# Optimization experiments

Measured on AMD Instinct MI355X. Metric: run time of the kernel, lower is better.

## Reference

```python
import jax, jax.numpy as jnp
import numpy as np

B, L, C = 8, 1_000_000, 4


def _spiral_size(length: int) -> int:
    # size = round(sqrt(L / (pi/4 * 0.7)) / 2) * 2 + 1  (odd, size^2 >= L)
    s = np.sqrt(length / (np.pi / 4.0 * 0.7))
    return int(np.round(s / 2.0)) * 2 + 1


def _spiral_perm(size: int, length: int):
    """Grid slot index for each signal position (first `length` of argsort(phi2))."""
    PI = jnp.float32(np.pi)
    rnge = jnp.arange(size, dtype=jnp.float32) - size / 2.0 + 0.5
    x1, x2 = jnp.meshgrid(rnge, rnge)  # 'xy' indexing, same as tf.meshgrid default
    r = jnp.sqrt(x1 * x1 + x2 * x2)
    phi = jnp.arccos(x1 / r)                      # NaN at center (0/0)
    phi = jnp.where(jnp.isnan(phi), 0.0, phi)
    phi = phi * jnp.sign(x2)
    phi = phi + jnp.where((x2 == 0.0) & (x1 < 0.0), PI, 0.0)
    phi2 = jnp.round(r) * 2.0 * PI + phi          # spiral ordering key
    return jnp.argsort(phi2.reshape(-1))[:length]


def setup_inputs() -> dict:
    key = jax.random.key(0)
    return {"inputs": jax.random.normal(key, (B, L, C), dtype=jnp.float32)}


def reference(inputs):
    b, l, c = inputs.shape
    size = _spiral_size(l)
    perm = _spiral_perm(size, l)  # [l] unique grid slots
    # One-pass scatter of the signal into the dense size*size spiral grid
    grid = jnp.zeros((b, size * size, c), dtype=inputs.dtype).at[:, perm, :].set(inputs)
    return grid.reshape(b, size, size, c)
```

## Files before the change

kernel.cpp:

```cpp
#include <hip/hip_runtime.h>
#include <cstdint>

#define SIZE 1349
#define HALF 674
#define N2 (SIZE*SIZE)
#define LSIG 1000000
#define NB 8
#define GRID_RINGS 954
#define CAP 5376
#define MBUCKET 2048

__device__ __forceinline__ int isqrt_i(int n) {
    int s = (int)sqrtf((float)n);
    while (s > 0 && s * s > n) s--;
    while ((s + 1) * (s + 1) <= n) s++;
    return s;
}

__device__ __forceinline__ int row_interval(int k, int y, int* xlo, int* xhi) {
    if (k == 0) { if (y == 0) { *xhi = 0; return 1; } return 0; }
    int yy = y * y;
    int B = k * (k + 1) - yy;
    if (B < 0) return 0;
    int h = isqrt_i(B);
    if (h > HALF) h = HALF;
    int A = k * (k - 1) + 1 - yy;
    *xhi = h;
    if (A <= 0) return 1;
    int f = isqrt_i(A);
    int lo = (f * f == A) ? f : f + 1;
    if (lo > h) return 0;
    *xlo = lo;
    return 2;
}

__device__ __forceinline__ uint32_t rowcnt(int k, int y) {
    int lo, hi;
    int kind = row_interval(k, y, &lo, &hi);
    if (kind == 0) return 0u;
    if (kind == 1) return (uint32_t)(2 * hi + 1);
    return (uint32_t)(2 * (hi - lo + 1));
}

__global__ void k_prep1(uint32_t* __restrict__ ringCount) {
    __shared__ uint32_t red[256];
    int k = blockIdx.x, t = threadIdx.x;
    int ymaxv = min(k, HALF);
    int nrows = 2 * ymaxv + 1;
    uint32_t s = 0;
    for (int i = t; i < nrows; i += 256) s += rowcnt(k, i - ymaxv);
    red[t] = s;
    __syncthreads();
    for (int d = 128; d > 0; d >>= 1) { if (t < d) red[t] += red[t + d]; __syncthreads(); }
    if (t == 0) ringCount[k] = red[0];
}

__global__ void k_prep2(const uint32_t* __restrict__ ringCount,
                        uint32_t* __restrict__ ringOffset) {
    __shared__ uint32_t s[1024];
    int t = threadIdx.x;
    uint32_t mine = (t < GRID_RINGS) ? ringCount[t] : 0u;
    s[t] = mine;
    __syncthreads();
    for (int d = 1; d < 1024; d <<= 1) {
        uint32_t x = (t >= d) ? s[t - d] : 0u;
        __syncthreads();
        s[t] += x;
        __syncthreads();
    }
    if (t < GRID_RINGS) ringOffset[t] = s[t] - mine;
}

__device__ __forceinline__ int bucket_of(uint32_t kb, float tt) {
    const float PI_F = 3.14159265358979323846f;
    const float SC = 325.94932f;
    float p2 = __uint_as_float(kb);
    float u = (p2 - tt) + PI_F;
    int b = (int)(u * SC);
    return min(max(b, 0), MBUCKET - 1);
}

template<int PHASE>
__device__ __forceinline__ void enum_ring(int k, int ymaxv, float tt, int t,
                                          uint32_t* cnt, uint32_t* boff, uint64_t* T) {
#pragma clang fp contract(off)
    const float PI_F = 3.14159265358979323846f;
    int ntask = 2 * (ymaxv + 1);
    for (int task = t; task < ntask; task += 1024) {
        int y = task >> 1, side = task & 1;
        int xlo = 0, xhi = 0;
        int kind = row_interval(k, y, &xlo, &xhi);
        if (kind == 0) continue;
        int xs, xe;
        if (side == 0) {
            xs = -xhi; xe = (kind == 1) ? -1 : -xlo;
            if (xe < xs) continue;
        } else {
            xs = (kind == 1) ? 0 : xlo; xe = xhi;
        }
        for (int x = xs; x <= xe; ++x) {
            uint32_t kp, kn = 0;
            if (y == 0) {
                float phi = (x < 0) ? PI_F : 0.0f;
                kp = __float_as_uint(tt + phi);
            } else {
                int nn = x * x + y * y;
                float rr = sqrtf((float)nn);
                float q = (float)x / rr;
                float ac = (float)::acos((double)q);
                kp = __float_as_uint(tt + ac);
                kn = __float_as_uint(tt - ac);
            }
            uint32_t gx = (uint32_t)(x + HALF);
            uint32_t gp = (uint32_t)(y + HALF) * SIZE + gx;
            int bp = bucket_of(kp, tt);
            if (PHASE == 0) atomicAdd(&cnt[bp], 1u);
            else { uint32_t p = atomicAdd(&boff[bp], 1u); T[p] = ((uint64_t)kp << 32) | gp; }
            if (y > 0) {
                uint32_t gn = (uint32_t)(HALF - y) * SIZE + gx;
                int bn = bucket_of(kn, tt);
                if (PHASE == 0) atomicAdd(&cnt[bn], 1u);
                else { uint32_t p = atomicAdd(&boff[bn], 1u); T[p] = ((uint64_t)kn << 32) | gn; }
            }
        }
    }
}

__global__ __launch_bounds__(1024) void k_rank(const uint32_t* __restrict__ ringOffset,
                                               const uint32_t* __restrict__ ringCount,
                                               uint32_t* __restrict__ rank) {
#pragma clang fp contract(off)
    __shared__ uint64_t T[CAP];
    __shared__ uint32_t cnt[MBUCKET];
    __shared__ uint32_t boff[MBUCKET];
    __shared__ uint32_t ps[1024];
    const float PI_F = 3.14159265358979323846f;
    int k = blockIdx.x, t = threadIdx.x;
    if (k == 0) { if (t == 0) rank[HALF * SIZE + HALF] = 0u; return; }
    int ymaxv = min(k, HALF);
    uint32_t off = ringOffset[k];
    int n = (int)ringCount[k];
    float tt = (2.0f * (float)k) * PI_F;

    cnt[2 * t] = 0u; cnt[2 * t + 1] = 0u;
    __syncthreads();

    enum_ring<0>(k, ymaxv, tt, t, cnt, boff, T);
    __syncthreads();

    uint32_t c0 = cnt[2 * t], c1 = cnt[2 * t + 1];
    uint32_t s = c0 + c1;
    ps[t] = s;
    __syncthreads();
    for (int d = 1; d < 1024; d <<= 1) {
        uint32_t x = (t >= d) ? ps[t - d] : 0u;
        __syncthreads();
        ps[t] += x;
        __syncthreads();
    }
    uint32_t excl = ps[t] - s;
    boff[2 * t] = excl;
    boff[2 * t + 1] = excl + c0;
    __syncthreads();

    enum_ring<1>(k, ymaxv, tt, t, cnt, boff, T);
    __syncthreads();

    for (int i = t; i < n; i += 1024) {
        uint64_t v = T[i];
        uint32_t kb = (uint32_t)(v >> 32);
        int b = bucket_of(kb, tt);
        uint32_t end = boff[b];
        uint32_t start = end - cnt[b];
        uint32_t c = 0;
        for (uint32_t j = start; j < end; ++j) c += (T[j] < v) ? 1u : 0u;
        rank[(uint32_t)v] = off + start + c;
    }
}

typedef float vfloat4 __attribute__((ext_vector_type(4)));

__global__ void k_gather(const vfloat4* __restrict__ in,
                         const uint32_t* __restrict__ rank,
                         vfloat4* __restrict__ out) {
    int g = blockIdx.x * blockDim.x + threadIdx.x;
    if (g >= N2) return;
    uint32_t q = rank[g];
    if (q < LSIG) {
#pragma unroll
        for (int b = 0; b < NB; ++b) {
            vfloat4 v = in[b * LSIG + (int)q];
            __builtin_nontemporal_store(v, &out[b * N2 + g]);
        }
    } else {
        vfloat4 z = {0.f, 0.f, 0.f, 0.f};
#pragma unroll
        for (int b = 0; b < NB; ++b)
            __builtin_nontemporal_store(z, &out[b * N2 + g]);
    }
}

extern "C" void kernel_launch(void* const* d_in, const int* in_sizes, int n_in,
                              void* d_out, int out_size, void* d_ws, size_t ws_size,
                              hipStream_t stream) {
    const float* in = (const float*)d_in[0];
    float* out = (float*)d_out;
    uint8_t* ws = (uint8_t*)d_ws;

    constexpr size_t RANK_OFF   = 0;
    constexpr size_t COUNT_OFF  = 7279616;
    constexpr size_t OFFSET_OFF = COUNT_OFF + 4096;

    uint32_t* rank       = (uint32_t*)(ws + RANK_OFF);
    uint32_t* ringCount  = (uint32_t*)(ws + COUNT_OFF);
    uint32_t* ringOffset = (uint32_t*)(ws + OFFSET_OFF);

    k_prep1<<<GRID_RINGS, 256, 0, stream>>>(ringCount);
    k_prep2<<<1, 1024, 0, stream>>>(ringCount, ringOffset);
    k_rank<<<GRID_RINGS, 1024, 0, stream>>>(ringOffset, ringCount, rank);

    int gblocks = (N2 + 255) / 256;
    k_gather<<<gblocks, 256, 0, stream>>>((const vfloat4*)in, rank, (vfloat4*)out);
}
```

Before: 397.9 us.

## Rank only rings covering the signal and skip rank reads beyond threshold

Ring enumeration and ranking now cover only the first 600 rings, and any ring whose offset already lies past the signal length exits early. Blocks are launched from the highest ring down so the long rings start first. The prefix pass computes a radius-squared threshold that the gather kernel checks before reading rank, so grid cells outside the filled disc write zeros without touching the stale rank buffer. The gather is also reorganised into 2D tiles. The aim is to cut the ranking work spent on unused outer rings and the rank loads for empty cells. This relies on the fixed 600-ring bound being large enough for this input size.

```diff
diff --git a/kernel.cpp b/kernel.cpp
--- a/kernel.cpp
+++ b/kernel.cpp
@@ -7,6 +7,7 @@
 #define LSIG 1000000
 #define NB 8
 #define GRID_RINGS 954
+#define RANK_RINGS 600
 #define CAP 5376
 #define MBUCKET 2048
 
@@ -56,10 +57,11 @@
 }
 
 __global__ void k_prep2(const uint32_t* __restrict__ ringCount,
-                        uint32_t* __restrict__ ringOffset) {
+                        uint32_t* __restrict__ ringOffset,
+                        uint32_t* __restrict__ nthresh) {
     __shared__ uint32_t s[1024];
     int t = threadIdx.x;
-    uint32_t mine = (t < GRID_RINGS) ? ringCount[t] : 0u;
+    uint32_t mine = (t < RANK_RINGS) ? ringCount[t] : 0u;
     s[t] = mine;
     __syncthreads();
     for (int d = 1; d < 1024; d <<= 1) {
@@ -68,7 +70,9 @@
         s[t] += x;
         __syncthreads();
     }
-    if (t < GRID_RINGS) ringOffset[t] = s[t] - mine;
+    if (t < RANK_RINGS) ringOffset[t] = s[t] - mine;
+    if (t >= 2 && t < RANK_RINGS && s[t - 1] >= LSIG && s[t - 2] < LSIG)
+        *nthresh = (uint32_t)(t * (t - 1) + 1);
 }
 
 __device__ __forceinline__ int bucket_of(uint32_t kb, float tt) {
@@ -135,10 +139,12 @@
     __shared__ uint32_t boff[MBUCKET];
     __shared__ uint32_t ps[1024];
     const float PI_F = 3.14159265358979323846f;
-    int k = blockIdx.x, t = threadIdx.x;
+    int k = (RANK_RINGS - 1) - blockIdx.x;
+    int t = threadIdx.x;
+    uint32_t off = ringOffset[k];
+    if (off >= LSIG) return;
     if (k == 0) { if (t == 0) rank[HALF * SIZE + HALF] = 0u; return; }
     int ymaxv = min(k, HALF);
-    uint32_t off = ringOffset[k];
     int n = (int)ringCount[k];
     float tt = (2.0f * (float)k) * PI_F;
 
@@ -180,12 +186,23 @@
 
 typedef float vfloat4 __attribute__((ext_vector_type(4)));
 
-__global__ void k_gather(const vfloat4* __restrict__ in,
-                         const uint32_t* __restrict__ rank,
-                         vfloat4* __restrict__ out) {
-    int g = blockIdx.x * blockDim.x + threadIdx.x;
-    if (g >= N2) return;
-    uint32_t q = rank[g];
+#define TW 32
+#define TH 8
+
+__global__ __launch_bounds__(256) void k_gather(const vfloat4* __restrict__ in,
+                                                const uint32_t* __restrict__ rank,
+                                                const uint32_t* __restrict__ nthresh,
+                                                vfloat4* __restrict__ out) {
+    int tx = threadIdx.x & (TW - 1);
+    int ty = threadIdx.x >> 5;
+    int col = blockIdx.x * TW + tx;
+    int row = blockIdx.y * TH + ty;
+    if (col >= SIZE || row >= SIZE) return;
+    int g = row * SIZE + col;
+    int dx = col - HALF, dy = row - HALF;
+    uint32_t n = (uint32_t)(dx * dx + dy * dy);
+    uint32_t q = 0xFFFFFFFFu;
+    if (n < *nthresh) q = rank[g];
     if (q < LSIG) {
 #pragma unroll
         for (int b = 0; b < NB; ++b) {
@@ -210,15 +227,17 @@
     constexpr size_t RANK_OFF   = 0;
     constexpr size_t COUNT_OFF  = 7279616;
     constexpr size_t OFFSET_OFF = COUNT_OFF + 4096;
+    constexpr size_t THRESH_OFF = OFFSET_OFF + 4096;
 
     uint32_t* rank       = (uint32_t*)(ws + RANK_OFF);
     uint32_t* ringCount  = (uint32_t*)(ws + COUNT_OFF);
     uint32_t* ringOffset = (uint32_t*)(ws + OFFSET_OFF);
-
-    k_prep1<<<GRID_RINGS, 256, 0, stream>>>(ringCount);
-    k_prep2<<<1, 1024, 0, stream>>>(ringCount, ringOffset);
-    k_rank<<<GRID_RINGS, 1024, 0, stream>>>(ringOffset, ringCount, rank);
-
-    int gblocks = (N2 + 255) / 256;
-    k_gather<<<gblocks, 256, 0, stream>>>((const vfloat4*)in, rank, (vfloat4*)out);
-}
+    uint32_t* nthresh    = (uint32_t*)(ws + THRESH_OFF);
+
+    k_prep1<<<RANK_RINGS, 256, 0, stream>>>(ringCount);
+    k_prep2<<<1, 1024, 0, stream>>>(ringCount, ringOffset, nthresh);
+    k_rank<<<RANK_RINGS, 1024, 0, stream>>>(ringOffset, ringCount, rank);
+
+    dim3 gb((SIZE + TW - 1) / TW, (SIZE + TH - 1) / TH);
+    k_gather<<<gb, 256, 0, stream>>>((const vfloat4*)in, rank, nthresh, (vfloat4*)out);
+}
```

Result: no change. 394.0 us (-1.0%).
